# Kernel tuning notes

Hardware: AMD Instinct MI355X
Metric: run time of the kernel (lower is better)

Reference implementation:

```python
import jax, jax.numpy as jnp
import numpy as np

M = 262144      # number of input points
NF = 16         # features per point
MAX_RADII = np.array([1.0, 1.0, 1.0])
RADII_RES = 4
ANG_RES = np.array([1, 2, 4, 8])


def sample_concentric_ellipsoids():
    """Deterministic kernel structure QX [K=85, 3] (concentric ellipsoids)."""
    Q = []
    for k in range(RADII_RES):
        if k == 0:
            Q.append(np.zeros(3))
            continue
        radii = k / (RADII_RES - 1) * MAX_RADII
        m = int(ANG_RES[k])
        for i in range(m):
            a = i / m * np.pi
            for j in range(m):
                b = j / m * 2 * np.pi
                Q.append(np.array([
                    radii[0] * np.sin(a) * np.cos(b),
                    radii[1] * np.sin(a) * np.sin(b),
                    radii[2] * np.cos(a),
                ]))
    return np.asarray(Q, dtype=np.float32)


def setup_inputs() -> dict:
    key = jax.random.key(0)
    kx, kf = jax.random.split(key)
    X = jax.random.uniform(kx, (M, 3), dtype=jnp.float32)      # points in unit cube
    F = jax.random.normal(kf, (M, NF), dtype=jnp.float32)
    QX = jnp.asarray(sample_concentric_ellipsoids())            # [K, 3], K = 85
    K = QX.shape[0]
    omegaD = jnp.ones((K,), dtype=jnp.float32)   # trainable, init ones (as in build)
    omegaF = jnp.ones((NF,), dtype=jnp.float32)  # trainable, init ones (as in build)
    return {"X": X, "F": F, "QX": QX, "omegaD": omegaD, "omegaF": omegaF}


def reference(X, F, QX, omegaD, omegaF):
    # SUB[k, i, :] = X[i] - QX[k]                       -> [K, M, 3]
    SUB = X[None, :, :] - QX[:, None, :]
    QDun = jnp.sum(SUB * SUB, axis=2)                   # squared distances [K, M]
    QD = jnp.exp(QDun / (omegaD * omegaD)[:, None])     # [K, M]
    QF = omegaF * (QD @ F)                              # kernel feature matrix [K, NF]
    FxQFT = F @ QF.T                                    # [M, K]
    # FULL concatenation strategy: [F, F QF^T, F QF^T QF]
    return jnp.concatenate([F, FxQFT, FxQFT @ QF], axis=1)   # [M, NF + K + NF]
```

## Files before the change

kernel.cpp:

```cpp
#include <hip/hip_runtime.h>

#define KP    96
#define NF    16
#define NCOL  117
#define PBLK  (KP * NF)
#define NB1   1024

typedef __attribute__((ext_vector_type(8))) short bf16x8;
typedef __attribute__((ext_vector_type(4))) float f32x4;

__device__ __forceinline__ float fast_exp2(float x) {
#if __has_builtin(__builtin_amdgcn_exp2f)
    return __builtin_amdgcn_exp2f(x);
#else
    float r;
    asm volatile("v_exp_f32 %0, %1" : "=v"(r) : "v"(x));
    return r;
#endif
}

__device__ __forceinline__ unsigned short f2bf(float f) {
    unsigned int u = __float_as_uint(f);
    u += 0x7FFFu + ((u >> 16) & 1u);
    return (unsigned short)(u >> 16);
}

__device__ __forceinline__ unsigned int pk_bf16(float lo, float hi) {
    unsigned int r;
    asm("v_cvt_pk_bf16_f32 %0, %1, %2" : "=v"(r) : "v"(lo), "v"(hi));
    return r;
}

__global__ __launch_bounds__(384) void k1_partial(
    const float* __restrict__ X, const float* __restrict__ F,
    const float* __restrict__ QX, const float* __restrict__ omegaD,
    int K, int ntile, float* __restrict__ partial)
{
    __shared__ float xs[2][4 * 32];
    __shared__ unsigned short fsb[2][32 * 18];

    const int tid  = threadIdx.x;
    const int lane = tid & 63;
    const int wv   = __builtin_amdgcn_readfirstlane(tid >> 6);
    const int kbase = wv * 16;
    const int m = lane & 15;
    const int g = lane >> 4;

    const int k = kbase + m;
    float qs0 = 0.f, qs1 = 0.f, qs2 = 0.f, cc = -3.0e8f, ss = 0.f;
    if (k < K) {
        const float qx = QX[k * 3 + 0];
        const float qy = QX[k * 3 + 1];
        const float qz = QX[k * 3 + 2];
        const float w  = omegaD[k];
        ss  = 1.4426950408889634f / (w * w);
        qs0 = 2.f * ss * qx; qs1 = 2.f * ss * qy; qs2 = 2.f * ss * qz;
        cc  = ss * (qx * qx + qy * qy + qz * qz);
    }

    f32x4 acc = {0.f, 0.f, 0.f, 0.f};

#define STAGE(BUF, TILE)                                                        \
    do {                                                                        \
        const int pbase_ = (TILE) * 32;                                         \
        for (int idx = tid; idx < 512; idx += 384) {                            \
            const int p_ = idx >> 4, n_ = idx & 15;                             \
            fsb[BUF][p_ * 18 + n_] = f2bf(F[(size_t)(pbase_ + p_) * NF + n_]);  \
        }                                                                       \
        if (tid < 32) {                                                         \
            const float x0_ = X[(pbase_ + tid) * 3 + 0];                        \
            const float x1_ = X[(pbase_ + tid) * 3 + 1];                        \
            const float x2_ = X[(pbase_ + tid) * 3 + 2];                        \
            xs[BUF][tid]      = x0_;                                            \
            xs[BUF][32 + tid] = x1_;                                            \
            xs[BUF][64 + tid] = x2_;                                            \
            xs[BUF][96 + tid] = x0_ * x0_ + x1_ * x1_ + x2_ * x2_;              \
        }                                                                       \
    } while (0)

    int t = blockIdx.x;
    int cur = 0;
    if (t < ntile) STAGE(0, t);
    __syncthreads();

    while (t < ntile) {
        const int tn = t + gridDim.x;
        float e[8];
        unsigned short bs[8];
#pragma unroll
        for (int i = 0; i < 8; ++i) {
            const int p = g * 8 + i;
            const float x0 = xs[cur][p], x1 = xs[cur][32 + p];
            const float x2 = xs[cur][64 + p], xn2 = xs[cur][96 + p];
            float h = fmaf(xn2, ss, cc);
            h = fmaf(-x0, qs0, h);
            h = fmaf(-x1, qs1, h);
            h = fmaf(-x2, qs2, h);
            e[i] = fast_exp2(h);
            bs[i] = fsb[cur][p * 18 + m];
        }
        if (tn < ntile) STAGE(cur ^ 1, tn);

        union { bf16x8 v; unsigned int u[4]; } af, bf;
#pragma unroll
        for (int j = 0; j < 4; ++j) {
            af.u[j] = pk_bf16(e[2 * j], e[2 * j + 1]);
            bf.u[j] = (unsigned int)bs[2 * j] | ((unsigned int)bs[2 * j + 1] << 16);
        }
        acc = __builtin_amdgcn_mfma_f32_16x16x32_bf16(af.v, bf.v, acc, 0, 0, 0);

        __syncthreads();
        cur ^= 1;
        t = tn;
    }
#undef STAGE

    float* pb = partial + (size_t)blockIdx.x * PBLK;
#pragma unroll
    for (int r = 0; r < 4; ++r) {
        const int krow = kbase + g * 4 + r;
        pb[krow * NF + m] = acc[r];
    }
}

__global__ __launch_bounds__(512) void k1_reduce(
    const float* __restrict__ partial, const float* __restrict__ omegaF,
    int nb, float* __restrict__ QF)
{
    const int k = blockIdx.x, tid = threadIdx.x;
    const int f = tid & 15, g = tid >> 4;
    const float* base = partial + k * NF + f;
    float s0 = 0.f, s1 = 0.f, s2 = 0.f, s3 = 0.f;
    float s4 = 0.f, s5 = 0.f, s6 = 0.f, s7 = 0.f;
    int b = g;
    for (; b + 224 < nb; b += 256) {
        s0 += base[(size_t)(b +   0) * PBLK];
        s1 += base[(size_t)(b +  32) * PBLK];
        s2 += base[(size_t)(b +  64) * PBLK];
        s3 += base[(size_t)(b +  96) * PBLK];
        s4 += base[(size_t)(b + 128) * PBLK];
        s5 += base[(size_t)(b + 160) * PBLK];
        s6 += base[(size_t)(b + 192) * PBLK];
        s7 += base[(size_t)(b + 224) * PBLK];
    }
    for (; b < nb; b += 32) s0 += base[(size_t)b * PBLK];
    const float s = ((s0 + s1) + (s2 + s3)) + ((s4 + s5) + (s6 + s7));

    __shared__ float red[32][17];
    red[g][f] = s;
    __syncthreads();
    if (tid < 16) {
        float t = 0.f;
#pragma unroll
        for (int g2 = 0; g2 < 32; ++g2) t += red[g2][tid];
        QF[k * NF + tid] = t * omegaF[tid];
    }
}

__global__ __launch_bounds__(256, 4) void k2_out(
    const float* __restrict__ F, const float* __restrict__ QFb,
    float* __restrict__ out)
{
    __shared__ __align__(16) float row[2][32 * NCOL];
    __shared__ __align__(16) float qf[85 * 16];
    __shared__ float b2[256];

    const int tid = threadIdx.x;
    const int q = tid & 31, pp = tid >> 5;

    for (int i = tid; i < 85 * 16; i += 256) qf[i] = QFb[i];
    __syncthreads();
    {
        const int u = tid & 15, v = tid >> 4;
        float s = 0.f;
        for (int k = 0; k < 85; ++k) s += qf[k * 16 + v] * qf[k * 16 + u];
        b2[tid] = s;
    }
    __syncthreads();

    float qr[3][NF];
#pragma unroll
    for (int j = 0; j < 3; ++j) {
        const int k = q + 32 * j;
        if (k < 85) {
#pragma unroll
            for (int u2 = 0; u2 < NF; ++u2) qr[j][u2] = qf[k * 16 + u2];
        } else {
#pragma unroll
            for (int u2 = 0; u2 < NF; ++u2) qr[j][u2] = 0.f;
        }
    }
    float b2c[NF];
#pragma unroll
    for (int v = 0; v < NF; ++v) b2c[v] = b2[v * 16 + (q & 15)];

    const int chunk = blockIdx.x * 256;
#pragma unroll 2
    for (int st = 0; st < 8; ++st) {
        const int sbase = chunk + st * 32;
        float* bufp = row[st & 1];
        float fr[NF];
        {
            const float4* Fv = reinterpret_cast<const float4*>(F + (size_t)(sbase + pp) * NF);
            const float4 t0 = Fv[0], t1 = Fv[1], t2 = Fv[2], t3 = Fv[3];
            fr[0]=t0.x; fr[1]=t0.y; fr[2]=t0.z; fr[3]=t0.w;
            fr[4]=t1.x; fr[5]=t1.y; fr[6]=t1.z; fr[7]=t1.w;
            fr[8]=t2.x; fr[9]=t2.y; fr[10]=t2.z; fr[11]=t2.w;
            fr[12]=t3.x; fr[13]=t3.y; fr[14]=t3.z; fr[15]=t3.w;
        }
#pragma unroll
        for (int it = 0; it < 4; ++it) {
            float4 n0, n1, n2, n3;
            if (it < 3) {
                const float4* Fv = reinterpret_cast<const float4*>(
                    F + (size_t)(sbase + (it + 1) * 8 + pp) * NF);
                n0 = Fv[0]; n1 = Fv[1]; n2 = Fv[2]; n3 = Fv[3];
            }
            float* rp = &bufp[(it * 8 + pp) * NCOL];
#pragma unroll
            for (int j = 0; j < 3; ++j) {
                const int k = q + 32 * j;
                float t = 0.f;
#pragma unroll
                for (int u2 = 0; u2 < NF; ++u2) t += fr[u2] * qr[j][u2];
                if (k < 85) rp[16 + k] = t;
            }
            if (q == 0) {
#pragma unroll
                for (int u2 = 0; u2 < NF; ++u2) rp[u2] = fr[u2];
            }
            if (q < 16) {
                float g = 0.f;
#pragma unroll
                for (int v = 0; v < NF; ++v) g += fr[v] * b2c[v];
                rp[101 + q] = g;
            }
            if (it < 3) {
                fr[0]=n0.x; fr[1]=n0.y; fr[2]=n0.z; fr[3]=n0.w;
                fr[4]=n1.x; fr[5]=n1.y; fr[6]=n1.z; fr[7]=n1.w;
                fr[8]=n2.x; fr[9]=n2.y; fr[10]=n2.z; fr[11]=n2.w;
                fr[12]=n3.x; fr[13]=n3.y; fr[14]=n3.z; fr[15]=n3.w;
            }
        }
        __syncthreads();
        {
            float4* dst = reinterpret_cast<float4*>(out + (size_t)sbase * NCOL);
            const float4* src = reinterpret_cast<const float4*>(bufp);
            for (int t2 = tid; t2 < (32 * NCOL) / 4; t2 += 256) dst[t2] = src[t2];
        }
    }
}

extern "C" void kernel_launch(void* const* d_in, const int* in_sizes, int n_in,
                              void* d_out, int out_size, void* d_ws, size_t ws_size,
                              hipStream_t stream)
{
    const float* X      = (const float*)d_in[0];
    const float* F      = (const float*)d_in[1];
    const float* QX     = (const float*)d_in[2];
    const float* omegaD = (const float*)d_in[3];
    const float* omegaF = (const float*)d_in[4];
    float* out = (float*)d_out;

    const int M = in_sizes[0] / 3;
    const int K = in_sizes[3];
    const int ntile = M / 32;

    int nb = (int)((ws_size / sizeof(float) - PBLK) / PBLK);
    if (nb > NB1) nb = NB1;
    if (nb > ntile) nb = ntile;
    if (nb < 1) nb = 1;

    float* partial = (float*)d_ws;
    float* QFbuf   = partial + (size_t)nb * PBLK;

    hipLaunchKernelGGL(k1_partial, dim3(nb), dim3(384), 0, stream,
                       X, F, QX, omegaD, K, ntile, partial);
    hipLaunchKernelGGL(k1_reduce, dim3(KP), dim3(512), 0, stream,
                       partial, omegaF, nb, QFbuf);
    hipLaunchKernelGGL(k2_out, dim3(M / 256), dim3(256), 0, stream,
                       F, QFbuf, out);
}
```

Baseline: 61.58 us.

## Fuse QF reduction into output kernel with a global flag barrier

Drops the separate reduce kernel. The first 96 blocks of the output kernel each reduce one row of the partial sums into QF and bump a global atomic counter. All blocks spin with sleeps until the counter reaches 96, with a fallback that makes a block reduce all rows itself on timeout. This removes one kernel launch and its gap, but risks spin stalls if the reducer blocks are not scheduled early, and the fallback does a lot of redundant reading.

```diff
diff --git a/kernel.cpp b/kernel.cpp
--- a/kernel.cpp
+++ b/kernel.cpp
@@ -34,12 +34,15 @@
 __global__ __launch_bounds__(384) void k1_partial(
     const float* __restrict__ X, const float* __restrict__ F,
     const float* __restrict__ QX, const float* __restrict__ omegaD,
-    int K, int ntile, float* __restrict__ partial)
+    int K, int ntile, float* __restrict__ partial,
+    unsigned int* __restrict__ flag)
 {
     __shared__ float xs[2][4 * 32];
     __shared__ unsigned short fsb[2][32 * 18];
 
     const int tid  = threadIdx.x;
+    if (blockIdx.x == 0 && tid == 0) flag[0] = 0u;
+
     const int lane = tid & 63;
     const int wv   = __builtin_amdgcn_readfirstlane(tid >> 6);
     const int kbase = wv * 16;
@@ -123,57 +126,76 @@
     }
 }
 
-__global__ __launch_bounds__(512) void k1_reduce(
-    const float* __restrict__ partial, const float* __restrict__ omegaF,
-    int nb, float* __restrict__ QF)
-{
-    const int k = blockIdx.x, tid = threadIdx.x;
-    const int f = tid & 15, g = tid >> 4;
-    const float* base = partial + k * NF + f;
-    float s0 = 0.f, s1 = 0.f, s2 = 0.f, s3 = 0.f;
-    float s4 = 0.f, s5 = 0.f, s6 = 0.f, s7 = 0.f;
-    int b = g;
-    for (; b + 224 < nb; b += 256) {
-        s0 += base[(size_t)(b +   0) * PBLK];
-        s1 += base[(size_t)(b +  32) * PBLK];
-        s2 += base[(size_t)(b +  64) * PBLK];
-        s3 += base[(size_t)(b +  96) * PBLK];
-        s4 += base[(size_t)(b + 128) * PBLK];
-        s5 += base[(size_t)(b + 160) * PBLK];
-        s6 += base[(size_t)(b + 192) * PBLK];
-        s7 += base[(size_t)(b + 224) * PBLK];
-    }
-    for (; b < nb; b += 32) s0 += base[(size_t)b * PBLK];
-    const float s = ((s0 + s1) + (s2 + s3)) + ((s4 + s5) + (s6 + s7));
-
-    __shared__ float red[32][17];
-    red[g][f] = s;
-    __syncthreads();
-    if (tid < 16) {
-        float t = 0.f;
-#pragma unroll
-        for (int g2 = 0; g2 < 32; ++g2) t += red[g2][tid];
-        QF[k * NF + tid] = t * omegaF[tid];
-    }
-}
-
 __global__ __launch_bounds__(256, 4) void k2_out(
-    const float* __restrict__ F, const float* __restrict__ QFb,
+    const float* __restrict__ F, const float* __restrict__ partial,
+    const float* __restrict__ omegaF, int nb,
+    float* __restrict__ QF, unsigned int* __restrict__ flag,
     float* __restrict__ out)
 {
     __shared__ __align__(16) float row[2][32 * NCOL];
     __shared__ __align__(16) float qf[85 * 16];
     __shared__ float b2[256];
+    __shared__ float reds[16][17];
+    __shared__ int ready;
 
     const int tid = threadIdx.x;
     const int q = tid & 31, pp = tid >> 5;
 
-    for (int i = tid; i < 85 * 16; i += 256) qf[i] = QFb[i];
+#define ROW_REDUCE(KROW, DST)                                                   \
+    do {                                                                        \
+        const int f_ = tid & 15, gg_ = tid >> 4;                                \
+        const float* base_ = partial + (KROW) * NF + f_;                        \
+        float s0 = 0.f, s1 = 0.f, s2 = 0.f, s3 = 0.f;                           \
+        int b_ = gg_;                                                           \
+        for (; b_ + 48 < nb; b_ += 64) {                                        \
+            s0 += base_[(size_t)(b_ +  0) * PBLK];                              \
+            s1 += base_[(size_t)(b_ + 16) * PBLK];                              \
+            s2 += base_[(size_t)(b_ + 32) * PBLK];                              \
+            s3 += base_[(size_t)(b_ + 48) * PBLK];                              \
+        }                                                                       \
+        for (; b_ < nb; b_ += 16) s0 += base_[(size_t)b_ * PBLK];               \
+        reds[gg_][f_] = (s0 + s1) + (s2 + s3);                                  \
+        __syncthreads();                                                        \
+        if (tid < 16) {                                                         \
+            float t_ = 0.f;                                                     \
+            _Pragma("unroll")                                                   \
+            for (int g2_ = 0; g2_ < 16; ++g2_) t_ += reds[g2_][tid];            \
+            DST;                                                                \
+        }                                                                       \
+        __syncthreads();                                                        \
+    } while (0)
+
+    if (blockIdx.x < KP) {
+        const int kk = blockIdx.x;
+        ROW_REDUCE(kk, QF[kk * NF + tid] = t_ * omegaF[tid]);
+        __threadfence();
+        if (tid == 0) atomicAdd(flag, 1u);
+    }
+
+    if (tid == 0) {
+        int it = 0;
+        while (atomicAdd(flag, 0u) < (unsigned int)KP) {
+            __builtin_amdgcn_s_sleep(8);
+            if (++it > 5000) break;
+        }
+        ready = (atomicAdd(flag, 0u) >= (unsigned int)KP) ? 1 : 0;
+        __threadfence();
+    }
     __syncthreads();
+
+    if (ready) {
+        for (int i = tid; i < 85 * 16; i += 256) qf[i] = QF[i];
+    } else {
+        for (int kk = 0; kk < 85; ++kk)
+            ROW_REDUCE(kk, qf[kk * 16 + tid] = t_ * omegaF[tid]);
+    }
+    __syncthreads();
+#undef ROW_REDUCE
+
     {
         const int u = tid & 15, v = tid >> 4;
         float s = 0.f;
-        for (int k = 0; k < 85; ++k) s += qf[k * 16 + v] * qf[k * 16 + u];
+        for (int kk = 0; kk < 85; ++kk) s += qf[kk * 16 + v] * qf[kk * 16 + u];
         b2[tid] = s;
     }
     __syncthreads();
@@ -181,10 +203,10 @@
     float qr[3][NF];
 #pragma unroll
     for (int j = 0; j < 3; ++j) {
-        const int k = q + 32 * j;
-        if (k < 85) {
-#pragma unroll
-            for (int u2 = 0; u2 < NF; ++u2) qr[j][u2] = qf[k * 16 + u2];
+        const int kk = q + 32 * j;
+        if (kk < 85) {
+#pragma unroll
+            for (int u2 = 0; u2 < NF; ++u2) qr[j][u2] = qf[kk * 16 + u2];
         } else {
 #pragma unroll
             for (int u2 = 0; u2 < NF; ++u2) qr[j][u2] = 0.f;
@@ -219,11 +241,11 @@
             float* rp = &bufp[(it * 8 + pp) * NCOL];
 #pragma unroll
             for (int j = 0; j < 3; ++j) {
-                const int k = q + 32 * j;
+                const int kk = q + 32 * j;
                 float t = 0.f;
 #pragma unroll
                 for (int u2 = 0; u2 < NF; ++u2) t += fr[u2] * qr[j][u2];
-                if (k < 85) rp[16 + k] = t;
+                if (kk < 85) rp[16 + kk] = t;
             }
             if (q == 0) {
 #pragma unroll
@@ -266,18 +288,17 @@
     const int K = in_sizes[3];
     const int ntile = M / 32;
 
-    int nb = (int)((ws_size / sizeof(float) - PBLK) / PBLK);
+    int nb = (int)((ws_size / sizeof(float) - PBLK - 16) / PBLK);
     if (nb > NB1) nb = NB1;
     if (nb > ntile) nb = ntile;
     if (nb < 1) nb = 1;
 
     float* partial = (float*)d_ws;
     float* QFbuf   = partial + (size_t)nb * PBLK;
+    unsigned int* flag = (unsigned int*)(QFbuf + PBLK);
 
     hipLaunchKernelGGL(k1_partial, dim3(nb), dim3(384), 0, stream,
-                       X, F, QX, omegaD, K, ntile, partial);
-    hipLaunchKernelGGL(k1_reduce, dim3(KP), dim3(512), 0, stream,
-                       partial, omegaF, nb, QFbuf);
+                       X, F, QX, omegaD, K, ntile, partial, flag);
     hipLaunchKernelGGL(k2_out, dim3(M / 256), dim3(256), 0, stream,
-                       F, QFbuf, out);
-}
+                       F, partial, omegaF, nb, QFbuf, flag, out);
+}
```

After: 93.91 us. 52.5% more time.
